# Performance work log

Hardware: AMD Instinct MI355X
Metric: run time of the kernel (lower is better)

The kernel has to match this reference:

```python
import jax, jax.numpy as jnp
import numpy as np

D = 768          # model dim (ViT-Base)
H = 12           # num heads
DH = 64          # head dim
DFF = 4 * D      # mlp hidden
SMAX = 1024      # max sequence length in the packed batch
LENS = np.array([1024, 896, 768, 640, 512, 448, 256, 64], dtype=np.int32)
TOTAL = int(LENS.sum())  # 4608
LN_EPS = 1e-6
NEG = -1e30


def _ln(x, w, b):
    mu = jnp.mean(x, axis=-1, keepdims=True)
    var = jnp.mean(jnp.square(x - mu), axis=-1, keepdims=True)
    return (x - mu) * jax.lax.rsqrt(var + LN_EPS) * w + b


def setup_inputs() -> dict:
    key = jax.random.key(0)
    ks = jax.random.split(key, 16)
    s = 0.02
    cu = jnp.asarray(np.concatenate([[0], np.cumsum(LENS)]).astype(np.int32))
    return {
        "x": jax.random.normal(ks[0], (TOTAL, D), jnp.float32),
        "norm1_w": jnp.ones((D,), jnp.float32),
        "norm1_b": jnp.zeros((D,), jnp.float32),
        "qkv_w": jax.random.normal(ks[1], (3 * D, D), jnp.float32) * s,
        "qkv_b": jnp.zeros((3 * D,), jnp.float32),
        "proj_w": jax.random.normal(ks[2], (D, D), jnp.float32) * s,
        "proj_b": jnp.zeros((D,), jnp.float32),
        "ls1_gamma": jax.random.normal(ks[3], (D,), jnp.float32) * 0.1,
        "norm2_w": jnp.ones((D,), jnp.float32),
        "norm2_b": jnp.zeros((D,), jnp.float32),
        "fc1_w": jax.random.normal(ks[4], (DFF, D), jnp.float32) * s,
        "fc1_b": jnp.zeros((DFF,), jnp.float32),
        "fc2_w": jax.random.normal(ks[5], (D, DFF), jnp.float32) * s,
        "fc2_b": jnp.zeros((D,), jnp.float32),
        "ls2_gamma": jax.random.normal(ks[6], (D,), jnp.float32) * 0.1,
        "cu_seqlens": cu,
    }


def reference(x, norm1_w, norm1_b, qkv_w, qkv_b, proj_w, proj_b, ls1_gamma,
              norm2_w, norm2_b, fc1_w, fc1_b, fc2_w, fc2_b, ls2_gamma,
              cu_seqlens):
    total = x.shape[0]
    B = cu_seqlens.shape[0] - 1
    tok = jnp.arange(total)
    seg = jnp.searchsorted(cu_seqlens[1:], tok, side="right")  # [Total]
    pos = tok - cu_seqlens[seg]                                 # [Total]
    lens = cu_seqlens[1:] - cu_seqlens[:-1]                     # [B]

    # --- attention branch ---
    xn = _ln(x, norm1_w, norm1_b)
    qkv = (xn @ qkv_w.T + qkv_b).reshape(total, 3, H, DH)
    q, k, v = qkv[:, 0], qkv[:, 1], qkv[:, 2]                   # [Total,H,DH]

    # pad packed ragged tokens to [B, SMAX, H, DH]
    def pad(t):
        return jnp.zeros((B, SMAX, H, DH), t.dtype).at[seg, pos].set(t)
    qp, kp, vp = pad(q), pad(k), pad(v)

    valid = jnp.arange(SMAX)[None, :] < lens[:, None]           # [B,SMAX]
    scores = jnp.einsum("bqhd,bkhd->bhqk", qp, kp) * (DH ** -0.5)
    scores = jnp.where(valid[:, None, None, :], scores, NEG)
    attn = jax.nn.softmax(scores, axis=-1)
    out = jnp.einsum("bhqk,bkhd->bqhd", attn, vp)
    out = out[seg, pos].reshape(total, D)                       # back to packed

    attn_out = out @ proj_w.T + proj_b
    x = x + ls1_gamma * attn_out

    # --- mlp branch ---
    xn2 = _ln(x, norm2_w, norm2_b)
    h = jax.nn.gelu(xn2 @ fc1_w.T + fc1_b, approximate=False)
    h = h @ fc2_w.T + fc2_b
    return x + ls2_gamma * h
```

## Files before the change

### kernel.cpp

```cpp
#include <hip/hip_runtime.h>
#include <hip/hip_bf16.h>
#include <stdint.h>

#define D 768
#define HEADS 12
#define DHEAD 64
#define DFF 3072
#define TOTAL 4608
#define NSEG 8

typedef __bf16 bf16;
typedef __bf16 bf16x8 __attribute__((ext_vector_type(8)));
typedef __bf16 bf16x4 __attribute__((ext_vector_type(4)));
typedef float f32x4 __attribute__((ext_vector_type(4)));

__device__ __forceinline__ void gld_lds16(const void* g, void* l) {
  __builtin_amdgcn_global_load_lds(
      (const __attribute__((address_space(1))) void*)g,
      (__attribute__((address_space(3))) void*)(uintptr_t)l, 16, 0, 0);
}

__global__ __launch_bounds__(256) void cvt_all_kernel(
    const float* __restrict__ a, const float* __restrict__ b,
    const float* __restrict__ c, const float* __restrict__ d,
    bf16* __restrict__ out, int nA, int nAB, int nABC, int nTot) {
  int i = blockIdx.x * blockDim.x + threadIdx.x;
  if (i >= nTot) return;
  const float* src;
  int j;
  if (i < nA) { src = a; j = i; }
  else if (i < nAB) { src = b; j = i - nA; }
  else if (i < nABC) { src = c; j = i - nAB; }
  else { src = d; j = i - nABC; }
  float4 v = ((const float4*)src)[j];
  bf16x4 o;
  o[0] = (bf16)v.x; o[1] = (bf16)v.y; o[2] = (bf16)v.z; o[3] = (bf16)v.w;
  ((bf16x4*)out)[i] = o;
}

__global__ __launch_bounds__(256) void ln_kernel(
    const float* __restrict__ x, const float* __restrict__ w,
    const float* __restrict__ b, bf16* __restrict__ out) {
  __shared__ float red[8];
  int row = blockIdx.x;
  const float* xr = x + (size_t)row * D;
  int t = threadIdx.x;
  float v[3];
  float s = 0.f, s2 = 0.f;
#pragma unroll
  for (int j = 0; j < 3; j++) {
    v[j] = xr[t + 256 * j];
    s += v[j]; s2 += v[j] * v[j];
  }
#pragma unroll
  for (int m = 1; m <= 32; m <<= 1) {
    s += __shfl_xor(s, m);
    s2 += __shfl_xor(s2, m);
  }
  int wave = t >> 6, lane = t & 63;
  if (lane == 0) { red[wave] = s; red[4 + wave] = s2; }
  __syncthreads();
  s = red[0] + red[1] + red[2] + red[3];
  s2 = red[4] + red[5] + red[6] + red[7];
  float mu = s * (1.f / 768.f);
  float var = s2 * (1.f / 768.f) - mu * mu;
  float rstd = rsqrtf(var + 1e-6f);
#pragma unroll
  for (int j = 0; j < 3; j++) {
    int c = t + 256 * j;
    out[(size_t)row * D + c] = (bf16)((v[j] - mu) * rstd * w[c] + b[c]);
  }
}

__device__ __forceinline__ float fast_gelu(float v) {
  float u = v * (0.7978845608f + 0.0356774081f * v * v);
  float e = exp2f(2.8853900818f * u);
  float th = 1.f - 2.f * __builtin_amdgcn_rcpf(1.f + e);
  return 0.5f * v * (1.f + th);
}

template <int MODE, int TN, int BK, int GX, int GY>
__global__ __launch_bounds__(512, 4) void gemm_kernel(
    const bf16* __restrict__ A, const bf16* __restrict__ W,
    const float* __restrict__ bias, const float* __restrict__ res,
    const float* __restrict__ gamma, bf16* __restrict__ outb,
    float* __restrict__ outf, int N, int K) {
  constexpr int WNW = (TN == 128) ? 4 : 2;
  constexpr int WMW = 8 / WNW;
  constexpr int MI = 128 / 16 / WMW;
  constexpr int NJ = TN / 16 / WNW;
  constexpr int KH = BK / 32;
  constexpr int CG = BK / 8;
  constexpr int SH = 0;
  constexpr int LPR = BK / 8;
  constexpr int RS = 64 / LPR;
  constexpr int RA = 128 / 8;
  constexpr int RB = TN / 8;
  __shared__ __align__(16) bf16 As[2][128 * BK];
  __shared__ __align__(16) bf16 Bs[2][TN * BK];

  const int g = blockIdx.x;
  const int xc = g & 7, q = g >> 3;
  const int bx = q % GX, by = xc + 8 * (q / GX);
  if (by >= GY) return;
  const int m0 = by * 128, n0 = bx * TN;

  const int t = threadIdx.x, wave = t >> 6, lane = t & 63;
  const int quad = lane >> 4, l16 = lane & 15;
  const int wm = (wave % WMW) * (MI * 16), wn = (wave / WMW) * (NJ * 16);

  const int ar = lane / LPR, ac = lane % LPR;
  const int acg = ac ^ (((wave * RA + ar) >> SH) & (CG - 1));
  const int bcg = ac ^ (((wave * RB + ar) >> SH) & (CG - 1));
  const bf16* gA = A + (size_t)(m0 + wave * RA + ar) * K + acg * 8;
  const bf16* gB = W + (size_t)(n0 + wave * RB + ar) * K + bcg * 8;

  auto stage = [&](int buf) {
#pragma unroll
    for (int n = 0; n < RA / RS; n++)
      gld_lds16(gA + (size_t)n * RS * K, &As[buf][(wave * RA + n * RS) * BK]);
#pragma unroll
    for (int n = 0; n < RB / RS; n++)
      gld_lds16(gB + (size_t)n * RS * K, &Bs[buf][(wave * RB + n * RS) * BK]);
    gA += BK; gB += BK;
  };

  stage(0);

  f32x4 acc[MI][NJ] = {};
  int cur = 0;
  for (int k0 = 0; k0 < K; k0 += BK) {
    __syncthreads();
    if (k0 + BK < K) stage(cur ^ 1);
    const bf16* as = As[cur];
    const bf16* bs = Bs[cur];
    bf16x8 af[KH][MI], bg[KH][NJ];
#pragma unroll
    for (int kh = 0; kh < KH; kh++) {
#pragma unroll
      for (int i = 0; i < MI; i++) {
        int R = wm + i * 16 + l16;
        af[kh][i] = *(const bf16x8*)&as[R * BK + 8 * ((kh * 4 + quad) ^ ((R >> SH) & (CG - 1)))];
      }
#pragma unroll
      for (int j = 0; j < NJ; j++) {
        int R = wn + j * 16 + l16;
        bg[kh][j] = *(const bf16x8*)&bs[R * BK + 8 * ((kh * 4 + quad) ^ ((R >> SH) & (CG - 1)))];
      }
    }
#pragma unroll
    for (int kh = 0; kh < KH; kh++)
#pragma unroll
      for (int i = 0; i < MI; i++)
#pragma unroll
        for (int j = 0; j < NJ; j++)
          acc[i][j] = __builtin_amdgcn_mfma_f32_16x16x32_bf16(af[kh][i], bg[kh][j], acc[i][j], 0, 0, 0);
    cur ^= 1;
  }

#pragma unroll
  for (int i = 0; i < MI; i++)
#pragma unroll
    for (int j = 0; j < NJ; j++)
#pragma unroll
      for (int r = 0; r < 4; r++) {
        int row = m0 + wm + i * 16 + quad * 4 + r;
        int col = n0 + wn + j * 16 + l16;
        float v = acc[i][j][r] + bias[col];
        if (MODE == 0) {
          outb[(size_t)row * N + col] = (bf16)v;
        } else if (MODE == 1) {
          outf[(size_t)row * N + col] = res[(size_t)row * N + col] + gamma[col] * v;
        } else {
          outb[(size_t)row * N + col] = (bf16)fast_gelu(v);
        }
      }
}

#define KCH 8
#define QT2 52

__global__ __launch_bounds__(256) void attn_kernel(
    const bf16* __restrict__ qkv, const int* __restrict__ cu,
    bf16* __restrict__ attn, float* __restrict__ Opart,
    float* __restrict__ lpart) {
  __shared__ __align__(16) bf16 Ks[64][72];
  __shared__ __align__(16) bf16 VTs[64][64];

  const int qt = blockIdx.x, h = blockIdx.y, ch = blockIdx.z;
  const int tok0 = qt * 64;
  int b = 0;
  while (cu[b + 1] <= tok0) b++;
  const int s0 = cu[b], S = cu[b + 1] - s0;

  const int ntile = S >> 6;
  const int nchunk = (ntile + KCH - 1) / KCH;
  if (ch >= nchunk) return;
  const int t0 = ch * KCH;
  const int t1 = (t0 + KCH < ntile) ? t0 + KCH : ntile;

  const int t = threadIdx.x, wave = t >> 6, lane = t & 63;
  const int quad = lane >> 4, l16 = lane & 15;

  const size_t qrow = (size_t)(tok0 + wave * 16 + l16) * (3 * D) + h * 64;
  const bf16x8 bq0 = *(const bf16x8*)&qkv[qrow + quad * 8];
  const bf16x8 bq1 = *(const bf16x8*)&qkv[qrow + 32 + quad * 8];

  const int srow = t >> 2, sc0 = (t & 3) * 16;
  const size_t kbase = (size_t)(s0 + srow) * (3 * D) + h * 64 + sc0 + D;
  const int vr0 = (t & 15) * 4, vd0 = (t >> 4) * 4;
  const size_t vbase = (size_t)(s0 + vr0) * (3 * D) + h * 64 + vd0 + 2 * D;
  const int kB0 = ((vr0 >> 5) << 5) | (((vr0 >> 2) & 3) << 3) | (((vr0 >> 4) & 1) << 2);

  bf16x8 kr0 = *(const bf16x8*)&qkv[kbase + (size_t)t0 * 64 * (3 * D)];
  bf16x8 kr1 = *(const bf16x8*)&qkv[kbase + (size_t)t0 * 64 * (3 * D) + 8];
  bf16x4 vp[4];
#pragma unroll
  for (int i = 0; i < 4; i++)
    vp[i] = *(const bf16x4*)&qkv[vbase + (size_t)t0 * 64 * (3 * D) + (size_t)i * (3 * D)];

  f32x4 Oacc[4] = {};
  float li = 0.f;
  const float SC = 0.125f * 1.44269504089f;
  const int vsw = (l16 & 7) * 8;

  for (int it = t0; it < t1; it++) {
    __syncthreads();
    *(bf16x8*)&Ks[srow][sc0] = kr0;
    *(bf16x8*)&Ks[srow][sc0 + 8] = kr1;
#pragma unroll
    for (int j = 0; j < 4; j++) {
      int d = vd0 + j;
      bf16x4 w;
      w[0] = vp[0][j]; w[1] = vp[1][j]; w[2] = vp[2][j]; w[3] = vp[3][j];
      *(bf16x4*)&VTs[d][kB0 ^ ((d & 7) * 8)] = w;
    }
    __syncthreads();

    if (it + 1 < t1) {
      const size_t koff = kbase + (size_t)(it + 1) * 64 * (3 * D);
      const size_t voff = vbase + (size_t)(it + 1) * 64 * (3 * D);
      kr0 = *(const bf16x8*)&qkv[koff];
      kr1 = *(const bf16x8*)&qkv[koff + 8];
#pragma unroll
      for (int i = 0; i < 4; i++)
        vp[i] = *(const bf16x4*)&qkv[voff + (size_t)i * (3 * D)];
    }

    f32x4 sac[4];
#pragma unroll
    for (int nt = 0; nt < 4; nt++) {
      bf16x8 ak0 = *(const bf16x8*)&Ks[nt * 16 + l16][quad * 8];
      bf16x8 ak1 = *(const bf16x8*)&Ks[nt * 16 + l16][32 + quad * 8];
      f32x4 z = {};
      z = __builtin_amdgcn_mfma_f32_16x16x32_bf16(ak0, bq0, z, 0, 0, 0);
      sac[nt] = __builtin_amdgcn_mfma_f32_16x16x32_bf16(ak1, bq1, z, 0, 0, 0);
    }

    bf16x8 bv0, bv1;
    float ls = 0.f;
#pragma unroll
    for (int r = 0; r < 4; r++) {
      float e0 = exp2f(sac[0][r] * SC);
      float e1 = exp2f(sac[1][r] * SC);
      float e2 = exp2f(sac[2][r] * SC);
      float e3 = exp2f(sac[3][r] * SC);
      ls += (e0 + e1) + (e2 + e3);
      bv0[r] = (bf16)e0; bv0[4 + r] = (bf16)e1;
      bv1[r] = (bf16)e2; bv1[4 + r] = (bf16)e3;
    }
    li += ls;

#pragma unroll
    for (int dt = 0; dt < 4; dt++) {
      bf16x8 av0 = *(const bf16x8*)&VTs[dt * 16 + l16][(quad * 8) ^ vsw];
      bf16x8 av1 = *(const bf16x8*)&VTs[dt * 16 + l16][(32 + quad * 8) ^ vsw];
      Oacc[dt] = __builtin_amdgcn_mfma_f32_16x16x32_bf16(av0, bv0, Oacc[dt], 0, 0, 0);
      Oacc[dt] = __builtin_amdgcn_mfma_f32_16x16x32_bf16(av1, bv1, Oacc[dt], 0, 0, 0);
    }
  }

  li += __shfl_xor(li, 16);
  li += __shfl_xor(li, 32);
  const int q = wave * 16 + l16;

  if (nchunk == 1) {
    const float inv = 1.f / li;
#pragma unroll
    for (int dt = 0; dt < 4; dt++) {
      bf16x4 w;
#pragma unroll
      for (int r = 0; r < 4; r++) w[r] = (bf16)(Oacc[dt][r] * inv);
      *(bf16x4*)&attn[(size_t)(tok0 + q) * D + h * 64 + dt * 16 + quad * 4] = w;
    }
  } else {
    const int slot = (h * QT2 + qt) * 2 + ch;
    float* op = Opart + (size_t)slot * 4096;
#pragma unroll
    for (int dt = 0; dt < 4; dt++)
      *(f32x4*)&op[q * 64 + dt * 16 + quad * 4] = Oacc[dt];
    if (quad == 0) lpart[(size_t)slot * 64 + q] = li;
  }
}

__global__ __launch_bounds__(256) void attn_reduce_kernel(
    const float* __restrict__ Opart, const float* __restrict__ lpart,
    const int* __restrict__ cu, bf16* __restrict__ attn) {
  const int qt = blockIdx.x, h = blockIdx.y;
  const int tok0 = qt * 64;
  int b = 0;
  while (cu[b + 1] <= tok0) b++;
  const int ntile = (cu[b + 1] - cu[b]) >> 6;
  if (ntile <= KCH) return;

  const int t = threadIdx.x, q = t >> 2, c0 = (t & 3) * 16;
  const int slot0 = (h * QT2 + qt) * 2;
  const float li = lpart[(size_t)slot0 * 64 + q] + lpart[(size_t)(slot0 + 1) * 64 + q];
  const float inv = 1.f / li;
  const float* p0 = Opart + (size_t)slot0 * 4096 + q * 64 + c0;
  const float* p1 = p0 + 4096;
  bf16x8 o0, o1;
#pragma unroll
  for (int g = 0; g < 4; g++) {
    f32x4 a = *(const f32x4*)&p0[g * 4];
    f32x4 c = *(const f32x4*)&p1[g * 4];
#pragma unroll
    for (int r = 0; r < 4; r++) {
      bf16 v = (bf16)((a[r] + c[r]) * inv);
      if (g < 2) o0[g * 4 + r] = v; else o1[(g - 2) * 4 + r] = v;
    }
  }
  const size_t ob = (size_t)(tok0 + q) * D + h * 64 + c0;
  *(bf16x8*)&attn[ob] = o0;
  *(bf16x8*)&attn[ob + 8] = o1;
}

extern "C" void kernel_launch(void* const* d_in, const int* in_sizes, int n_in,
                              void* d_out, int out_size, void* d_ws,
                              size_t ws_size, hipStream_t stream) {
  const float* x       = (const float*)d_in[0];
  const float* norm1_w = (const float*)d_in[1];
  const float* norm1_b = (const float*)d_in[2];
  const float* qkv_w   = (const float*)d_in[3];
  const float* qkv_b   = (const float*)d_in[4];
  const float* proj_w  = (const float*)d_in[5];
  const float* proj_b  = (const float*)d_in[6];
  const float* ls1     = (const float*)d_in[7];
  const float* norm2_w = (const float*)d_in[8];
  const float* norm2_b = (const float*)d_in[9];
  const float* fc1_w   = (const float*)d_in[10];
  const float* fc1_b   = (const float*)d_in[11];
  const float* fc2_w   = (const float*)d_in[12];
  const float* fc2_b   = (const float*)d_in[13];
  const float* ls2     = (const float*)d_in[14];
  const int*   cu      = (const int*)d_in[15];
  float* out = (float*)d_out;

  char* ws = (char*)d_ws;
  size_t off = 0;
  auto alloc = [&](size_t bytes) {
    void* p = ws + off;
    off += (bytes + 255) & ~(size_t)255;
    return p;
  };
  bf16* w_qkv  = (bf16*)alloc((size_t)3 * D * D * 2);
  bf16* w_proj = (bf16*)alloc((size_t)D * D * 2);
  bf16* w_fc1  = (bf16*)alloc((size_t)DFF * D * 2);
  bf16* w_fc2  = (bf16*)alloc((size_t)D * DFF * 2);
  bf16* xn     = (bf16*)alloc((size_t)TOTAL * D * 2);
  bf16* qkv    = (bf16*)alloc((size_t)TOTAL * 3 * D * 2);
  bf16* attnb  = (bf16*)alloc((size_t)TOTAL * D * 2);
  float* x1    = (float*)alloc((size_t)TOTAL * D * 4);
  float* Opart = (float*)alloc((size_t)QT2 * HEADS * 2 * 4096 * 4);
  float* lpart = (float*)alloc((size_t)QT2 * HEADS * 2 * 64 * 4);
  bf16* hbuf   = qkv;

  {
    int nA   = 3 * D * D / 4;
    int nAB  = nA + D * D / 4;
    int nABC = nAB + DFF * D / 4;
    int nTot = nABC + D * DFF / 4;
    cvt_all_kernel<<<(nTot + 255) / 256, 256, 0, stream>>>(
        qkv_w, proj_w, fc1_w, fc2_w, w_qkv, nA, nAB, nABC, nTot);
  }

  ln_kernel<<<TOTAL, 256, 0, stream>>>(x, norm1_w, norm1_b, xn);

  constexpr int GY = TOTAL / 128;
  constexpr int GYP = ((GY + 7) / 8) * 8;

  gemm_kernel<0, 128, 64, 18, GY><<<18 * GYP, 512, 0, stream>>>(
      xn, w_qkv, qkv_b, nullptr, nullptr, qkv, nullptr, 3 * D, D);

  dim3 ga(TOTAL / 64, HEADS, 2);
  attn_kernel<<<ga, 256, 0, stream>>>(qkv, cu, attnb, Opart, lpart);
  attn_reduce_kernel<<<dim3(QT2, HEADS), 256, 0, stream>>>(Opart, lpart, cu, attnb);

  gemm_kernel<1, 64, 64, 12, GY><<<12 * GYP, 512, 0, stream>>>(
      attnb, w_proj, proj_b, x, ls1, nullptr, x1, D, D);

  ln_kernel<<<TOTAL, 256, 0, stream>>>(x1, norm2_w, norm2_b, xn);

  gemm_kernel<2, 128, 64, 24, GY><<<24 * GYP, 512, 0, stream>>>(
      xn, w_fc1, fc1_b, nullptr, nullptr, hbuf, nullptr, DFF, D);

  gemm_kernel<1, 64, 64, 12, GY><<<12 * GYP, 512, 0, stream>>>(
      hbuf, w_fc2, fc2_b, x1, ls2, nullptr, out, D, DFF);
}
```

Baseline: 261.0 us.

## Switch GEMMs to 32x32 MFMA, split-K fc2, fuse weight cast with LN1

```diff
diff --git a/kernel.cpp b/kernel.cpp
--- a/kernel.cpp
+++ b/kernel.cpp
@@ -13,6 +13,7 @@
 typedef __bf16 bf16x8 __attribute__((ext_vector_type(8)));
 typedef __bf16 bf16x4 __attribute__((ext_vector_type(4)));
 typedef float f32x4 __attribute__((ext_vector_type(4)));
+typedef float f32x16 __attribute__((ext_vector_type(16)));
 
 __device__ __forceinline__ void gld_lds16(const void* g, void* l) {
   __builtin_amdgcn_global_load_lds(
@@ -20,22 +21,56 @@
       (__attribute__((address_space(3))) void*)(uintptr_t)l, 16, 0, 0);
 }
 
-__global__ __launch_bounds__(256) void cvt_all_kernel(
-    const float* __restrict__ a, const float* __restrict__ b,
-    const float* __restrict__ c, const float* __restrict__ d,
-    bf16* __restrict__ out, int nA, int nAB, int nABC, int nTot) {
-  int i = blockIdx.x * blockDim.x + threadIdx.x;
-  if (i >= nTot) return;
-  const float* src;
-  int j;
-  if (i < nA) { src = a; j = i; }
-  else if (i < nAB) { src = b; j = i - nA; }
-  else if (i < nABC) { src = c; j = i - nAB; }
-  else { src = d; j = i - nABC; }
-  float4 v = ((const float4*)src)[j];
-  bf16x4 o;
-  o[0] = (bf16)v.x; o[1] = (bf16)v.y; o[2] = (bf16)v.z; o[3] = (bf16)v.w;
-  ((bf16x4*)out)[i] = o;
+__global__ __launch_bounds__(256) void prep_kernel(
+    const float* __restrict__ x, const float* __restrict__ w,
+    const float* __restrict__ b, bf16* __restrict__ xn,
+    const float* __restrict__ wa, const float* __restrict__ wb,
+    const float* __restrict__ wc, const float* __restrict__ wd,
+    bf16* __restrict__ wout, int nA, int nAB, int nABC, int nTot) {
+  __shared__ float red[8];
+  const int t = threadIdx.x;
+  if (blockIdx.x >= TOTAL) {
+    int i = (blockIdx.x - TOTAL) * 256 + t;
+    if (i >= nTot) return;
+    const float* src;
+    int j;
+    if (i < nA) { src = wa; j = i; }
+    else if (i < nAB) { src = wb; j = i - nA; }
+    else if (i < nABC) { src = wc; j = i - nAB; }
+    else { src = wd; j = i - nABC; }
+    float4 v = ((const float4*)src)[j];
+    bf16x4 o;
+    o[0] = (bf16)v.x; o[1] = (bf16)v.y; o[2] = (bf16)v.z; o[3] = (bf16)v.w;
+    ((bf16x4*)wout)[i] = o;
+    return;
+  }
+  const int row = blockIdx.x;
+  const float* xr = x + (size_t)row * D;
+  float v[3];
+  float s = 0.f, s2 = 0.f;
+#pragma unroll
+  for (int j = 0; j < 3; j++) {
+    v[j] = xr[t + 256 * j];
+    s += v[j]; s2 += v[j] * v[j];
+  }
+#pragma unroll
+  for (int m = 1; m <= 32; m <<= 1) {
+    s += __shfl_xor(s, m);
+    s2 += __shfl_xor(s2, m);
+  }
+  int wave = t >> 6, lane = t & 63;
+  if (lane == 0) { red[wave] = s; red[4 + wave] = s2; }
+  __syncthreads();
+  s = red[0] + red[1] + red[2] + red[3];
+  s2 = red[4] + red[5] + red[6] + red[7];
+  float mu = s * (1.f / 768.f);
+  float var = s2 * (1.f / 768.f) - mu * mu;
+  float rstd = rsqrtf(var + 1e-6f);
+#pragma unroll
+  for (int j = 0; j < 3; j++) {
+    int c = t + 256 * j;
+    xn[(size_t)row * D + c] = (bf16)((v[j] - mu) * rstd * w[c] + b[c]);
+  }
 }
 
 __global__ __launch_bounds__(256) void ln_kernel(
@@ -79,7 +114,7 @@
   return 0.5f * v * (1.f + th);
 }
 
-template <int MODE, int TN, int BK, int GX, int GY>
+template <int MODE, int TN, int BK, int GX, int GY, int SPLIT = 0>
 __global__ __launch_bounds__(512, 4) void gemm_kernel(
     const bf16* __restrict__ A, const bf16* __restrict__ W,
     const float* __restrict__ bias, const float* __restrict__ res,
@@ -87,9 +122,9 @@
     float* __restrict__ outf, int N, int K) {
   constexpr int WNW = (TN == 128) ? 4 : 2;
   constexpr int WMW = 8 / WNW;
-  constexpr int MI = 128 / 16 / WMW;
-  constexpr int NJ = TN / 16 / WNW;
-  constexpr int KH = BK / 32;
+  constexpr int MI = 128 / 32 / WMW;
+  constexpr int NJ = TN / 32 / WNW;
+  constexpr int KH = BK / 16;
   constexpr int CG = BK / 8;
   constexpr int SH = 0;
   constexpr int LPR = BK / 8;
@@ -104,16 +139,19 @@
   const int bx = q % GX, by = xc + 8 * (q / GX);
   if (by >= GY) return;
   const int m0 = by * 128, n0 = bx * TN;
+  const int kz = SPLIT ? blockIdx.y : 0;
+  const int Keff = SPLIT ? (K >> 1) : K;
+  const int koff = kz * Keff;
 
   const int t = threadIdx.x, wave = t >> 6, lane = t & 63;
-  const int quad = lane >> 4, l16 = lane & 15;
-  const int wm = (wave % WMW) * (MI * 16), wn = (wave / WMW) * (NJ * 16);
+  const int l32 = lane & 31, hi = lane >> 5;
+  const int wm = (wave % WMW) * (MI * 32), wn = (wave / WMW) * (NJ * 32);
 
   const int ar = lane / LPR, ac = lane % LPR;
   const int acg = ac ^ (((wave * RA + ar) >> SH) & (CG - 1));
   const int bcg = ac ^ (((wave * RB + ar) >> SH) & (CG - 1));
-  const bf16* gA = A + (size_t)(m0 + wave * RA + ar) * K + acg * 8;
-  const bf16* gB = W + (size_t)(n0 + wave * RB + ar) * K + bcg * 8;
+  const bf16* gA = A + (size_t)(m0 + wave * RA + ar) * K + koff + acg * 8;
+  const bf16* gB = W + (size_t)(n0 + wave * RB + ar) * K + koff + bcg * 8;
 
   auto stage = [&](int buf) {
 #pragma unroll
@@ -127,34 +165,34 @@
 
   stage(0);
 
-  f32x4 acc[MI][NJ] = {};
+  f32x16 acc[MI][NJ] = {};
   int cur = 0;
-  for (int k0 = 0; k0 < K; k0 += BK) {
+  for (int k0 = 0; k0 < Keff; k0 += BK) {
     __syncthreads();
-    if (k0 + BK < K) stage(cur ^ 1);
+    if (k0 + BK < Keff) stage(cur ^ 1);
     const bf16* as = As[cur];
     const bf16* bs = Bs[cur];
     bf16x8 af[KH][MI], bg[KH][NJ];
 #pragma unroll
-    for (int kh = 0; kh < KH; kh++) {
+    for (int ks = 0; ks < KH; ks++) {
 #pragma unroll
       for (int i = 0; i < MI; i++) {
-        int R = wm + i * 16 + l16;
-        af[kh][i] = *(const bf16x8*)&as[R * BK + 8 * ((kh * 4 + quad) ^ ((R >> SH) & (CG - 1)))];
+        int R = wm + i * 32 + l32;
+        af[ks][i] = *(const bf16x8*)&as[R * BK + 8 * ((ks * 2 + hi) ^ ((R >> SH) & (CG - 1)))];
       }
 #pragma unroll
       for (int j = 0; j < NJ; j++) {
-        int R = wn + j * 16 + l16;
-        bg[kh][j] = *(const bf16x8*)&bs[R * BK + 8 * ((kh * 4 + quad) ^ ((R >> SH) & (CG - 1)))];
+        int R = wn + j * 32 + l32;
+        bg[ks][j] = *(const bf16x8*)&bs[R * BK + 8 * ((ks * 2 + hi) ^ ((R >> SH) & (CG - 1)))];
       }
     }
 #pragma unroll
-    for (int kh = 0; kh < KH; kh++)
+    for (int ks = 0; ks < KH; ks++)
 #pragma unroll
       for (int i = 0; i < MI; i++)
 #pragma unroll
         for (int j = 0; j < NJ; j++)
-          acc[i][j] = __builtin_amdgcn_mfma_f32_16x16x32_bf16(af[kh][i], bg[kh][j], acc[i][j], 0, 0, 0);
+          acc[i][j] = __builtin_amdgcn_mfma_f32_32x32x16_bf16(af[ks][i], bg[ks][j], acc[i][j], 0, 0, 0);
     cur ^= 1;
   }
 
@@ -163,18 +201,42 @@
 #pragma unroll
     for (int j = 0; j < NJ; j++)
 #pragma unroll
-      for (int r = 0; r < 4; r++) {
-        int row = m0 + wm + i * 16 + quad * 4 + r;
-        int col = n0 + wn + j * 16 + l16;
-        float v = acc[i][j][r] + bias[col];
-        if (MODE == 0) {
-          outb[(size_t)row * N + col] = (bf16)v;
-        } else if (MODE == 1) {
-          outf[(size_t)row * N + col] = res[(size_t)row * N + col] + gamma[col] * v;
-        } else {
-          outb[(size_t)row * N + col] = (bf16)fast_gelu(v);
+      for (int rg = 0; rg < 4; rg++)
+#pragma unroll
+        for (int r = 0; r < 4; r++) {
+          int row = m0 + wm + i * 32 + rg * 8 + hi * 4 + r;
+          int col = n0 + wn + j * 32 + l32;
+          float v = acc[i][j][rg * 4 + r];
+          if (MODE == 0) {
+            outb[(size_t)row * N + col] = (bf16)(v + bias[col]);
+          } else if (MODE == 1) {
+            outf[(size_t)row * N + col] =
+                res[(size_t)row * N + col] + gamma[col] * (v + bias[col]);
+          } else if (MODE == 2) {
+            outb[(size_t)row * N + col] = (bf16)fast_gelu(v + bias[col]);
+          } else {
+            outf[((size_t)kz * TOTAL + row) * N + col] = v;
+          }
         }
-      }
+}
+
+__global__ __launch_bounds__(256) void fc2_merge_kernel(
+    const float* __restrict__ p, const float* __restrict__ x1,
+    const float* __restrict__ bias, const float* __restrict__ gamma,
+    float* __restrict__ out) {
+  const int i4 = blockIdx.x * 256 + threadIdx.x;
+  const int col = (i4 * 4) % D;
+  const float4 a = ((const float4*)p)[i4];
+  const float4 b2 = ((const float4*)(p + (size_t)TOTAL * D))[i4];
+  const float4 xr = ((const float4*)x1)[i4];
+  const float4 bb = *(const float4*)&bias[col];
+  const float4 gg = *(const float4*)&gamma[col];
+  float4 o;
+  o.x = xr.x + gg.x * (a.x + b2.x + bb.x);
+  o.y = xr.y + gg.y * (a.y + b2.y + bb.y);
+  o.z = xr.z + gg.z * (a.z + b2.z + bb.z);
+  o.w = xr.w + gg.w * (a.w + b2.w + bb.w);
+  ((float4*)out)[i4] = o;
 }
 
 #define KCH 8
@@ -373,6 +435,7 @@
   float* x1    = (float*)alloc((size_t)TOTAL * D * 4);
   float* Opart = (float*)alloc((size_t)QT2 * HEADS * 2 * 4096 * 4);
   float* lpart = (float*)alloc((size_t)QT2 * HEADS * 2 * 64 * 4);
+  float* fc2p  = (float*)alloc((size_t)2 * TOTAL * D * 4);
   bf16* hbuf   = qkv;
 
   {
@@ -380,11 +443,10 @@
     int nAB  = nA + D * D / 4;
     int nABC = nAB + DFF * D / 4;
     int nTot = nABC + D * DFF / 4;
-    cvt_all_kernel<<<(nTot + 255) / 256, 256, 0, stream>>>(
-        qkv_w, proj_w, fc1_w, fc2_w, w_qkv, nA, nAB, nABC, nTot);
-  }
-
-  ln_kernel<<<TOTAL, 256, 0, stream>>>(x, norm1_w, norm1_b, xn);
+    prep_kernel<<<TOTAL + (nTot + 255) / 256, 256, 0, stream>>>(
+        x, norm1_w, norm1_b, xn, qkv_w, proj_w, fc1_w, fc2_w, w_qkv,
+        nA, nAB, nABC, nTot);
+  }
 
   constexpr int GY = TOTAL / 128;
   constexpr int GYP = ((GY + 7) / 8) * 8;
@@ -404,6 +466,8 @@
   gemm_kernel<2, 128, 64, 24, GY><<<24 * GYP, 512, 0, stream>>>(
       xn, w_fc1, fc1_b, nullptr, nullptr, hbuf, nullptr, DFF, D);
 
-  gemm_kernel<1, 64, 64, 12, GY><<<12 * GYP, 512, 0, stream>>>(
-      hbuf, w_fc2, fc2_b, x1, ls2, nullptr, out, D, DFF);
-}
+  gemm_kernel<3, 64, 64, 12, GY, 1><<<dim3(12 * GYP, 2), 512, 0, stream>>>(
+      hbuf, w_fc2, nullptr, nullptr, nullptr, nullptr, fc2p, D, DFF);
+  fc2_merge_kernel<<<TOTAL * D / 4 / 256, 256, 0, stream>>>(
+      fc2p, x1, fc2_b, ls2, out);
+}
```

After: 282.4 us. +8.2%, slower.
